# Kernel tuning notes

Measured on AMD Instinct MI355X. Metric: run time of the kernel, lower is better.

Reference implementation:

```python
import jax, jax.numpy as jnp
import numpy as np

N, D, K = 32768, 256, 2048
BETA = 0.25  # init arg beta, in [0,1) branch of the loss


def setup_inputs() -> dict:
    key = jax.random.key(0)
    k1, k2 = jax.random.split(key)
    x = jax.random.normal(k1, (N, D), dtype=jnp.float32)
    # mimics nn.Embedding init: uniform(-1/K, 1/K) then mean-centered
    cb = jax.random.uniform(k2, (K, D), dtype=jnp.float32, minval=-1.0 / K, maxval=1.0 / K)
    codebook = cb - cb.mean(axis=0)
    return {"x": x, "codebook": codebook}


def reference(x, codebook):
    # pairwise squared L2 distances: [N, K]
    dist = (
        jnp.sum(x * x, axis=1, keepdims=True)
        + jnp.sum(codebook * codebook, axis=1)
        - 2.0 * jnp.matmul(x, codebook.T)
    )
    encoding_inds = jnp.argmin(dist, axis=1)  # [N]
    # one-hot @ codebook == gather of nearest code vectors
    x_codebook = jnp.take(codebook, encoding_inds, axis=0)  # [N, D]
    # straight-through quantization
    x_quantized = x + jax.lax.stop_gradient(x_codebook - x)
    # VQ loss, beta in [0, 1) branch
    commit = jnp.mean((x - jax.lax.stop_gradient(x_codebook)) ** 2)
    embed = jnp.mean((x_codebook - jax.lax.stop_gradient(x)) ** 2)
    loss = BETA * commit + embed
    return x_quantized, loss
```

## Files before the change

### kernel.cpp

```cpp
#include <hip/hip_runtime.h>

#define N_ROWS 32768
#define DIM    256
#define KCODES 2048
#define CSCALE 4096.0f

typedef __attribute__((ext_vector_type(16))) float f32x16;
typedef __attribute__((ext_vector_type(4)))  unsigned int u32x4;
union frag16 { u32x4 v; long l[2]; };

__device__ __forceinline__ uint4 pack16(const float* s) {
    int a = __builtin_amdgcn_cvt_pk_fp8_f32(s[0],  s[1],  0, false);
    a     = __builtin_amdgcn_cvt_pk_fp8_f32(s[2],  s[3],  a, true);
    int b = __builtin_amdgcn_cvt_pk_fp8_f32(s[4],  s[5],  0, false);
    b     = __builtin_amdgcn_cvt_pk_fp8_f32(s[6],  s[7],  b, true);
    int c = __builtin_amdgcn_cvt_pk_fp8_f32(s[8],  s[9],  0, false);
    c     = __builtin_amdgcn_cvt_pk_fp8_f32(s[10], s[11], c, true);
    int d = __builtin_amdgcn_cvt_pk_fp8_f32(s[12], s[13], 0, false);
    d     = __builtin_amdgcn_cvt_pk_fp8_f32(s[14], s[15], d, true);
    uint4 o; o.x = a; o.y = b; o.z = c; o.w = d;
    return o;
}


__global__ void prep_cb(const float* __restrict__ cb, unsigned int* __restrict__ cbf8,
                        float* __restrict__ halfcn, float* __restrict__ loss) {
    const int t    = threadIdx.x;
    const int code = blockIdx.x * 4 + (t >> 6);
    const int s    = t & 63;
    if (blockIdx.x == 0 && t == 0) *loss = 0.0f;
    const int kc = s >> 4, d = (s >> 2) & 3, b4 = (s & 3) * 4;
    const int h = d >> 1, q = d & 1;
    const int k0 = kc * 64 + q * 32 + (b4 >> 3) * 16 + h * 8 + (b4 & 7);
    float4 v = *(const float4*)&cb[(size_t)code * DIM + k0];
    int pk = __builtin_amdgcn_cvt_pk_fp8_f32(v.x * CSCALE, v.y * CSCALE, 0, false);
    pk     = __builtin_amdgcn_cvt_pk_fp8_f32(v.z * CSCALE, v.w * CSCALE, pk, true);
    cbf8[(size_t)code * 64 + s] = (unsigned int)pk;
    float ssum = v.x * v.x + v.y * v.y + v.z * v.z + v.w * v.w;
    #pragma unroll
    for (int o = 32; o > 0; o >>= 1) ssum += __shfl_down(ssum, o, 64);
    if (s == 0) halfcn[code] = 0.5f * CSCALE * ssum;
}

__global__ __launch_bounds__(256, 2) void vq_fused(
        const float* __restrict__ x, const float* __restrict__ cb,
        const char* __restrict__ cbf8, const float* __restrict__ halfcn,
        float* __restrict__ out, float* __restrict__ loss) {
    __shared__ char mem[16384];

    const int t    = threadIdx.x;
    const int lane = t & 63;
    const int w    = t >> 6;
    const int l32  = lane & 31;
    const int h    = lane >> 5;
    const int row0 = blockIdx.x * 64;

    {
        const int r   = t >> 2;
        const int kc  = t & 3;
        const int key = (r >> 1) & 3;
        const float* src = x + (size_t)(row0 + r) * DIM + kc * 64;
        float buf[16];
        #pragma unroll
        for (int p = 0; p < 4; p++) {
            const int d = p ^ key, hh = d >> 1, qq = d & 1;
            #pragma unroll
            for (int j = 0; j < 4; j++) *(float4*)(buf + j * 4) =
                *(const float4*)(src + qq * 32 + (j >> 1) * 16 + hh * 8 + (j & 1) * 4);
            *(uint4*)(mem + kc * 4096 + r * 64 + p * 16) = pack16(buf);
        }
    }
    __syncthreads();

    const int key = (l32 >> 1) & 3;
    frag16 xf[2][4][2];
    #pragma unroll
    for (int rt = 0; rt < 2; rt++)
        #pragma unroll
        for (int kc = 0; kc < 4; kc++)
            #pragma unroll
            for (int q = 0; q < 2; q++)
                xf[rt][kc][q].v = *(const u32x4*)(mem + kc * 4096
                    + (rt * 32 + l32) * 64 + (((h * 2 + q) ^ key)) * 16);
    __syncthreads();

    frag16 cf[2][4][2];
    float  bias[2][16];
    {
        const char* cbase = cbf8 + (size_t)(w * 32 + l32) * DIM;
        #pragma unroll
        for (int kc = 0; kc < 4; kc++)
            #pragma unroll
            for (int q = 0; q < 2; q++)
                cf[0][kc][q].v = *(const u32x4*)(cbase + kc * 64 + (h * 2 + q) * 16);
        #pragma unroll
        for (int g4 = 0; g4 < 4; g4++)
            *(float4*)&bias[0][g4 * 4] = *(const float4*)&halfcn[w * 32 + g4 * 8 + 4 * h];
    }

    float mp[2] = {-3.0e38f, -3.0e38f};

    #pragma unroll 2
    for (int g = 0; g < 16; ++g) {
        const int cur = g & 1, nxt = cur ^ 1;
        if (g < 15) {
            const char* cbase = cbf8 + (size_t)((g + 1) * 128 + w * 32 + l32) * DIM;
            #pragma unroll
            for (int kc = 0; kc < 4; kc++)
                #pragma unroll
                for (int q = 0; q < 2; q++)
                    cf[nxt][kc][q].v = *(const u32x4*)(cbase + kc * 64 + (h * 2 + q) * 16);
            #pragma unroll
            for (int g4 = 0; g4 < 4; g4++)
                *(float4*)&bias[nxt][g4 * 4] =
                    *(const float4*)&halfcn[(g + 1) * 128 + w * 32 + g4 * 8 + 4 * h];
        }

        f32x16 acc[2];
        #pragma unroll
        for (int r = 0; r < 16; r++) { acc[0][r] = -bias[cur][r]; acc[1][r] = -bias[cur][r]; }

        #pragma unroll
        for (int kc = 0; kc < 4; kc++)
            #pragma unroll
            for (int q = 0; q < 2; q++)
                #pragma unroll
                for (int sl = 0; sl < 2; sl++)
                    #pragma unroll
                    for (int rt = 0; rt < 2; rt++)
                        acc[rt] = __builtin_amdgcn_mfma_f32_32x32x16_fp8_fp8(
                            cf[cur][kc][q].l[sl], xf[rt][kc][q].l[sl], acc[rt], 0, 0, 0);

        const unsigned codebase = (unsigned)(g * 128 + w * 32 + 4 * h);
        #pragma unroll
        for (int rt = 0; rt < 2; rt++) {
            float best = mp[rt];
            #pragma unroll
            for (int r = 0; r < 16; r++) {
                const unsigned code = codebase + (unsigned)((r & 3) + 8 * (r >> 2));
                const unsigned u = (__float_as_uint(acc[rt][r]) & 0xFFFFF800u) | code;
                best = fmaxf(best, __uint_as_float(u));
            }
            mp[rt] = best;
        }
    }

    #pragma unroll
    for (int rt = 0; rt < 2; rt++)
        mp[rt] = fmaxf(mp[rt], __shfl_xor(mp[rt], 32, 64));

    __syncthreads();
    float* red  = (float*)mem;
    int*   idxs = (int*)(mem + 1024);
    float* lred = (float*)(mem + 1280);

    if (h == 0) {
        red[(l32)      * 4 + w] = mp[0];
        red[(32 + l32) * 4 + w] = mp[1];
    }
    __syncthreads();
    if (t < 64) {
        float b0 = fmaxf(fmaxf(red[t * 4 + 0], red[t * 4 + 1]),
                         fmaxf(red[t * 4 + 2], red[t * 4 + 3]));
        idxs[t] = (int)(__float_as_uint(b0) & 2047u);
    }
    __syncthreads();

    float lsum = 0.0f;
    #pragma unroll 4
    for (int r = 0; r < 64; r++) {
        const int code = idxs[r];
        const float c  = cb[(size_t)code * DIM + t];
        const float xv = x[(size_t)(row0 + r) * DIM + t];
        out[(size_t)(row0 + r) * DIM + t] = c;
        const float d = xv - c;
        lsum += d * d;
    }
    #pragma unroll
    for (int o = 32; o > 0; o >>= 1) lsum += __shfl_down(lsum, o, 64);
    if (lane == 0) lred[w] = lsum;
    __syncthreads();
    if (t == 0) {
        const float scale = 1.25f / (float)((size_t)N_ROWS * DIM);
        atomicAdd(loss, (lred[0] + lred[1] + lred[2] + lred[3]) * scale);
    }
}

extern "C" void kernel_launch(void* const* d_in, const int* in_sizes, int n_in,
                              void* d_out, int out_size, void* d_ws, size_t ws_size,
                              hipStream_t stream) {
    const float* x  = (const float*)d_in[0];
    const float* cb = (const float*)d_in[1];
    float* out  = (float*)d_out;
    float* loss = out + (size_t)N_ROWS * DIM;

    char* ws = (char*)d_ws;
    unsigned int* cbf8 = (unsigned int*)ws;
    float* halfcn = (float*)(ws + (size_t)KCODES * 256);

    prep_cb<<<KCODES / 4, 256, 0, stream>>>(cb, cbf8, halfcn, loss);
    vq_fused<<<N_ROWS / 64, 256, 0, stream>>>(x, cb, (const char*)cbf8, halfcn, out, loss);
}
```

Before: 131.0 us.

## Repack fp8 codebook into per-group coalesced fragment layout and drop register double-buffering

The prep kernel now writes the fp8 codebook in a layout grouped by 32-code tiles, so each wave loads a fragment with a fully contiguous 16-byte-per-lane access (lane*16 + j*1024). This replaces the earlier strided per-code loads. The main loop now walks groups w+4i and no longer prefetches the next group into a second register buffer. That frees registers but exposes global load latency, which now depends on occupancy and the compiler's scheduling to hide.

```diff
diff --git a/kernel.cpp b/kernel.cpp
--- a/kernel.cpp
+++ b/kernel.cpp
@@ -29,13 +29,13 @@
     const int code = blockIdx.x * 4 + (t >> 6);
     const int s    = t & 63;
     if (blockIdx.x == 0 && t == 0) *loss = 0.0f;
-    const int kc = s >> 4, d = (s >> 2) & 3, b4 = (s & 3) * 4;
-    const int h = d >> 1, q = d & 1;
-    const int k0 = kc * 64 + q * 32 + (b4 >> 3) * 16 + h * 8 + (b4 & 7);
+    const int kc = s >> 4, q = (s >> 3) & 1, h = (s >> 2) & 1, d4 = s & 3;
+    const int k0 = kc * 64 + q * 32 + h * 8 + (d4 >> 1) * 16 + (d4 & 1) * 4;
     float4 v = *(const float4*)&cb[(size_t)code * DIM + k0];
     int pk = __builtin_amdgcn_cvt_pk_fp8_f32(v.x * CSCALE, v.y * CSCALE, 0, false);
     pk     = __builtin_amdgcn_cvt_pk_fp8_f32(v.z * CSCALE, v.w * CSCALE, pk, true);
-    cbf8[(size_t)code * 64 + s] = (unsigned int)pk;
+    const int g = code >> 5, cm = code & 31;
+    cbf8[(size_t)g * 2048 + (kc * 2 + q) * 256 + (h * 32 + cm) * 4 + d4] = (unsigned)pk;
     float ssum = v.x * v.x + v.y * v.y + v.z * v.z + v.w * v.w;
     #pragma unroll
     for (int o = 32; o > 0; o >>= 1) ssum += __shfl_down(ssum, o, 64);
@@ -84,41 +84,25 @@
                     + (rt * 32 + l32) * 64 + (((h * 2 + q) ^ key)) * 16);
     __syncthreads();
 
-    frag16 cf[2][4][2];
-    float  bias[2][16];
-    {
-        const char* cbase = cbf8 + (size_t)(w * 32 + l32) * DIM;
+    float mp[2] = {-3.0e38f, -3.0e38f};
+
+    for (int i = 0; i < 16; ++i) {
+        const int g = w + 4 * i;
+
+        frag16 cf[8];
+        const char* gbase = cbf8 + (size_t)g * 8192 + lane * 16;
         #pragma unroll
-        for (int kc = 0; kc < 4; kc++)
-            #pragma unroll
-            for (int q = 0; q < 2; q++)
-                cf[0][kc][q].v = *(const u32x4*)(cbase + kc * 64 + (h * 2 + q) * 16);
+        for (int j = 0; j < 8; j++)
+            cf[j].v = *(const u32x4*)(gbase + j * 1024);
+
+        float bias[16];
         #pragma unroll
         for (int g4 = 0; g4 < 4; g4++)
-            *(float4*)&bias[0][g4 * 4] = *(const float4*)&halfcn[w * 32 + g4 * 8 + 4 * h];
-    }
-
-    float mp[2] = {-3.0e38f, -3.0e38f};
-
-    #pragma unroll 2
-    for (int g = 0; g < 16; ++g) {
-        const int cur = g & 1, nxt = cur ^ 1;
-        if (g < 15) {
-            const char* cbase = cbf8 + (size_t)((g + 1) * 128 + w * 32 + l32) * DIM;
-            #pragma unroll
-            for (int kc = 0; kc < 4; kc++)
-                #pragma unroll
-                for (int q = 0; q < 2; q++)
-                    cf[nxt][kc][q].v = *(const u32x4*)(cbase + kc * 64 + (h * 2 + q) * 16);
-            #pragma unroll
-            for (int g4 = 0; g4 < 4; g4++)
-                *(float4*)&bias[nxt][g4 * 4] =
-                    *(const float4*)&halfcn[(g + 1) * 128 + w * 32 + g4 * 8 + 4 * h];
-        }
+            *(float4*)&bias[g4 * 4] = *(const float4*)&halfcn[g * 32 + g4 * 8 + 4 * h];
 
         f32x16 acc[2];
         #pragma unroll
-        for (int r = 0; r < 16; r++) { acc[0][r] = -bias[cur][r]; acc[1][r] = -bias[cur][r]; }
+        for (int r = 0; r < 16; r++) { acc[0][r] = -bias[r]; acc[1][r] = -bias[r]; }
 
         #pragma unroll
         for (int kc = 0; kc < 4; kc++)
@@ -129,9 +113,9 @@
                     #pragma unroll
                     for (int rt = 0; rt < 2; rt++)
                         acc[rt] = __builtin_amdgcn_mfma_f32_32x32x16_fp8_fp8(
-                            cf[cur][kc][q].l[sl], xf[rt][kc][q].l[sl], acc[rt], 0, 0, 0);
+                            cf[kc * 2 + q].l[sl], xf[rt][kc][q].l[sl], acc[rt], 0, 0, 0);
 
-        const unsigned codebase = (unsigned)(g * 128 + w * 32 + 4 * h);
+        const unsigned codebase = (unsigned)(g * 32 + 4 * h);
         #pragma unroll
         for (int rt = 0; rt < 2; rt++) {
             float best = mp[rt];
```

After: 126.3 us. -3.6%, faster.
